# Optimization experiments

Measured on AMD Instinct MI355X. Metric: run time of the kernel, lower is better.

Reference implementation:

```python
import jax, jax.numpy as jnp
import numpy as np

EPS_ATT = 1e-6
EPS_BN = 1e-5


def setup_inputs() -> dict:
    key = jax.random.key(0)
    ks = jax.random.split(key, 12)
    B, Cin_half, H, W = 16, 128, 96, 96
    Cin, Cout, Cqk = 2 * Cin_half, 256, 256 // 8
    inp = {
        'fsp': jax.random.normal(ks[0], (B, Cin_half, H, W), jnp.float32),
        'fcp': jax.random.normal(ks[1], (B, Cin_half, H, W), jnp.float32),
        # 1x1 conv of ConvBNReLU (bias=False): store as [out, in]
        'conv_w': jax.random.normal(ks[2], (Cout, Cin), jnp.float32) * (1.0 / np.sqrt(Cin)),
        'bn_scale': jax.random.normal(ks[3], (Cout,), jnp.float32) * 0.1 + 1.0,
        'bn_bias': jax.random.normal(ks[4], (Cout,), jnp.float32) * 0.1,
        'bn_mean': jax.random.normal(ks[5], (Cout,), jnp.float32) * 0.1,
        'bn_var': jax.random.uniform(ks[6], (Cout,), jnp.float32, 0.5, 1.5),
        'gamma': jnp.ones((1,), jnp.float32) * 0.5,  # attention residual scale
        'q_w': jax.random.normal(ks[7], (Cqk, Cout), jnp.float32) * (1.0 / np.sqrt(Cout)),
        'q_b': jnp.zeros((Cqk,), jnp.float32),
        'k_w': jax.random.normal(ks[8], (Cqk, Cout), jnp.float32) * (1.0 / np.sqrt(Cout)),
        'k_b': jnp.zeros((Cqk,), jnp.float32),
        'v_w': jax.random.normal(ks[9], (Cout, Cout), jnp.float32) * (1.0 / np.sqrt(Cout)),
        'v_b': jnp.zeros((Cout,), jnp.float32),
    }
    return inp


def _l2_norm(x):
    # x: [B, C, N]; normalize over channel dim (dim=-2), matching torch l2_norm
    return x / jnp.linalg.norm(x, axis=-2, keepdims=True)


def reference(fsp, fcp, conv_w, bn_scale, bn_bias, bn_mean, bn_var,
              gamma, q_w, q_b, k_w, k_b, v_w, v_b):
    x = jnp.concatenate([fsp, fcp], axis=1)  # [B, Cin, H, W]
    # 1x1 conv + BN (eval, running stats) + ReLU
    feat = jnp.einsum('bchw,oc->bohw', x, conv_w)
    inv_std = jax.lax.rsqrt(bn_var + EPS_BN)
    feat = (feat - bn_mean[:, None, None]) * (bn_scale * inv_std)[:, None, None] + bn_bias[:, None, None]
    feat = jax.nn.relu(feat)

    B, C, H, W = feat.shape
    N = H * W
    f = feat.reshape(B, C, N)
    Q = jnp.einsum('bcn,oc->bon', f, q_w) + q_b[:, None]  # [B, Cq, N]
    K = jnp.einsum('bcn,oc->bon', f, k_w) + k_b[:, None]
    V = jnp.einsum('bcn,oc->bon', f, v_w) + v_b[:, None]  # [B, C, N]

    Qn = _l2_norm(Q).transpose(0, 2, 1)  # [B, N, Cq]
    Kn = _l2_norm(K)                     # [B, Cq, N]

    tailor = 1.0 / (N + jnp.einsum('bnc,bc->bn', Qn, jnp.sum(Kn, axis=-1) + EPS_ATT))  # [B, N]
    value_sum = jnp.sum(V, axis=-1)[:, :, None]          # [B, C, 1]
    matrix = jnp.einsum('bmn,bcn->bmc', Kn, V)           # [B, Cq, C]
    matrix_sum = value_sum + jnp.einsum('bnm,bmc->bcn', Qn, matrix)  # [B, C, N]
    weight_value = (matrix_sum * tailor[:, None, :]).reshape(B, C, H, W)

    atten = feat + gamma[0] * weight_value
    return feat * atten + feat
```

## Files before the change

### kernel.cpp

```cpp
#include <hip/hip_runtime.h>


typedef short short8 __attribute__((ext_vector_type(8)));
typedef __bf16 bf16x8 __attribute__((ext_vector_type(8)));
typedef float f32x4 __attribute__((ext_vector_type(4)));

#define DEVFN static __device__ __forceinline__

static constexpr int NB = 16;
static constexpr int C = 256;
static constexpr int HW = 9216;
static constexpr float FN = 9216.0f;
static constexpr float EPS_ATT_C = 1e-6f;
static constexpr float EPS_BN_C = 1e-5f;

DEVFN unsigned short f2b(float f) {
  unsigned u = __float_as_uint(f);
  u += 0x7FFFu + ((u >> 16) & 1u);
  return (unsigned short)(u >> 16);
}
DEVFN float b2f(unsigned short s) { return __uint_as_float(((unsigned)s) << 16); }

DEVFN float featval(float v) { return v; }
DEVFN float featval(unsigned short v) { return b2f(v); }
DEVFN short featbits(float v) { return (short)f2b(v); }
DEVFN short featbits(unsigned short v) { return (short)v; }
DEVFN void feat_store(float* p, float v) { *p = v; }
DEVFN void feat_store(unsigned short* p, float v) { *p = f2b(v); }

DEVFN f32x4 mfma16(short8 a, short8 b, f32x4 c) {
  return __builtin_amdgcn_mfma_f32_16x16x32_bf16(
      __builtin_bit_cast(bf16x8, a), __builtin_bit_cast(bf16x8, b), c, 0, 0, 0);
}

__global__ __launch_bounds__(256) void k_prep(
    const float* __restrict__ conv_w, const float* __restrict__ bn_scale,
    const float* __restrict__ bn_bias, const float* __restrict__ bn_mean,
    const float* __restrict__ bn_var, const float* __restrict__ q_w,
    const float* __restrict__ k_w, const float* __restrict__ v_w,
    unsigned short* __restrict__ Abf, float* __restrict__ biasA,
    unsigned short* __restrict__ qwbf, unsigned short* __restrict__ kwbf,
    float* __restrict__ vwT, float* __restrict__ fsum, float* __restrict__ Ksum,
    float* __restrict__ KF) {
  int tid = blockIdx.x * 256 + threadIdx.x;
  int nth = gridDim.x * 256;
  for (int i = tid; i < 65536; i += nth) {
    int o = i >> 8;
    float sc = bn_scale[o] * rsqrtf(bn_var[o] + EPS_BN_C);
    Abf[i] = f2b(conv_w[i] * sc);
  }
  for (int i = tid; i < 256; i += nth) {
    float sc = bn_scale[i] * rsqrtf(bn_var[i] + EPS_BN_C);
    biasA[i] = bn_bias[i] - bn_mean[i] * sc;
  }
  for (int i = tid; i < 8192; i += nth) {
    qwbf[i] = f2b(q_w[i]);
    kwbf[i] = f2b(k_w[i]);
  }
  for (int i = tid; i < 65536; i += nth) {
    int c = i >> 8, cp = i & 255;
    vwT[cp * 256 + c] = v_w[i];
  }
  for (int i = tid; i < NB * 256; i += nth) fsum[i] = 0.f;
  for (int i = tid; i < NB * 32; i += nth) Ksum[i] = 0.f;
  for (int i = tid; i < NB * 32 * 256; i += nth) KF[i] = 0.f;
}

template <typename FT>
__global__ __launch_bounds__(256) void k_conv(
    const float* __restrict__ fsp, const float* __restrict__ fcp,
    const unsigned short* __restrict__ Abf, const float* __restrict__ biasA,
    FT* __restrict__ feat, float* __restrict__ fsum) {
  const int b = blockIdx.y;
  const int p0 = blockIdx.x * 64;
  const int tid = threadIdx.x;
  const int w = tid >> 6, lane = tid & 63, g = lane >> 4, li = lane & 15;

  f32x4 acc[4][4];
#pragma unroll
  for (int i = 0; i < 4; ++i)
#pragma unroll
    for (int j = 0; j < 4; ++j) acc[i][j] = f32x4{0.f, 0.f, 0.f, 0.f};

  const short* Ab = (const short*)Abf;

#pragma unroll 1
  for (int kk = 0; kk < 256; kk += 32) {
    short8 af[4];
#pragma unroll
    for (int i = 0; i < 4; ++i) {
      int o = w * 64 + i * 16 + li;
      af[i] = *(const short8*)(Ab + o * 256 + kk + g * 8);
    }
    const float* src = (kk < 128) ? (fsp + ((size_t)b * 128 + kk) * HW)
                                  : (fcp + ((size_t)b * 128 + (kk - 128)) * HW);
    short8 bfr[4];
#pragma unroll
    for (int j = 0; j < 4; ++j) {
      const float* sp = src + (size_t)g * 8 * HW + p0 + j * 16 + li;
#pragma unroll
      for (int jj = 0; jj < 8; ++jj) bfr[j][jj] = (short)f2b(sp[(size_t)jj * HW]);
    }
#pragma unroll
    for (int i = 0; i < 4; ++i)
#pragma unroll
      for (int j = 0; j < 4; ++j)
        acc[i][j] = mfma16(af[i], bfr[j], acc[i][j]);
  }

  FT* fb = feat + (size_t)b * C * HW;
#pragma unroll
  for (int i = 0; i < 4; ++i) {
#pragma unroll
    for (int r = 0; r < 4; ++r) {
      int o = w * 64 + i * 16 + g * 4 + r;
      float bias = biasA[o];
      float s = 0.f;
#pragma unroll
      for (int j = 0; j < 4; ++j) {
        int p = p0 + j * 16 + li;
        float v = fmaxf(acc[i][j][r] + bias, 0.f);
        feat_store(&fb[(size_t)o * HW + p], v);
        s += v;
      }
      s += __shfl_xor(s, 1); s += __shfl_xor(s, 2);
      s += __shfl_xor(s, 4); s += __shfl_xor(s, 8);
      if (li == 0) atomicAdd(&fsum[b * 256 + o], s);
    }
  }
}

template <typename FT>
__global__ __launch_bounds__(256) void k_qk(
    const FT* __restrict__ feat, const unsigned short* __restrict__ qwbf,
    const unsigned short* __restrict__ kwbf, const float* __restrict__ q_b,
    const float* __restrict__ k_b, unsigned short* __restrict__ QnT,
    unsigned short* __restrict__ Kn, float* __restrict__ Ksum) {
  const int b = blockIdx.y;
  const int tid = threadIdx.x;
  const int w = tid >> 6, lane = tid & 63, g = lane >> 4, li = lane & 15;
  const int p0 = blockIdx.x * 256 + w * 64;

  const FT* fs = feat + (size_t)b * C * HW;
  const short* qw = (const short*)qwbf;
  const short* kw = (const short*)kwbf;

  f32x4 aq[4][2], ak[2][4];
#pragma unroll
  for (int t = 0; t < 4; ++t)
#pragma unroll
    for (int m = 0; m < 2; ++m) {
      aq[t][m] = f32x4{0.f, 0.f, 0.f, 0.f};
      ak[m][t] = f32x4{0.f, 0.f, 0.f, 0.f};
    }

#pragma unroll 1
  for (int kk = 0; kk < 256; kk += 32) {
    short8 ft[4];
#pragma unroll
    for (int t = 0; t < 4; ++t) {
      const FT* f8 = fs + (size_t)(kk + g * 8) * HW + p0 + t * 16 + li;
#pragma unroll
      for (int jj = 0; jj < 8; ++jj) ft[t][jj] = featbits(f8[(size_t)jj * HW]);
    }
    short8 qf[2], kf[2];
#pragma unroll
    for (int m = 0; m < 2; ++m) {
      qf[m] = *(const short8*)(qw + (m * 16 + li) * 256 + kk + g * 8);
      kf[m] = *(const short8*)(kw + (m * 16 + li) * 256 + kk + g * 8);
    }
#pragma unroll
    for (int t = 0; t < 4; ++t)
#pragma unroll
      for (int m = 0; m < 2; ++m)
        aq[t][m] = mfma16(ft[t], qf[m], aq[t][m]);
#pragma unroll
    for (int m = 0; m < 2; ++m)
#pragma unroll
      for (int t = 0; t < 4; ++t)
        ak[m][t] = mfma16(kf[m], ft[t], ak[m][t]);
  }

  float qb0 = q_b[li], qb1 = q_b[16 + li];
#pragma unroll
  for (int t = 0; t < 4; ++t) {
#pragma unroll
    for (int r = 0; r < 4; ++r) {
      float v0 = aq[t][0][r] + qb0;
      float v1 = aq[t][1][r] + qb1;
      float ss = v0 * v0 + v1 * v1;
      ss += __shfl_xor(ss, 1); ss += __shfl_xor(ss, 2);
      ss += __shfl_xor(ss, 4); ss += __shfl_xor(ss, 8);
      float sc = 1.0f / sqrtf(ss);
      int p = p0 + t * 16 + g * 4 + r;
      unsigned short* qp = QnT + ((size_t)b * HW + p) * 32;
      qp[li] = f2b(v0 * sc);
      qp[16 + li] = f2b(v1 * sc);
    }
  }

  float kb[2][4];
#pragma unroll
  for (int mi = 0; mi < 2; ++mi)
#pragma unroll
    for (int r = 0; r < 4; ++r) kb[mi][r] = k_b[mi * 16 + g * 4 + r];

  float ks[2][4];
#pragma unroll
  for (int mi = 0; mi < 2; ++mi)
#pragma unroll
    for (int r = 0; r < 4; ++r) ks[mi][r] = 0.f;

#pragma unroll
  for (int t = 0; t < 4; ++t) {
    float v[2][4];
    float ss = 0.f;
#pragma unroll
    for (int mi = 0; mi < 2; ++mi)
#pragma unroll
      for (int r = 0; r < 4; ++r) {
        v[mi][r] = ak[mi][t][r] + kb[mi][r];
        ss += v[mi][r] * v[mi][r];
      }
    ss += __shfl_xor(ss, 16); ss += __shfl_xor(ss, 32);
    float sc = 1.0f / sqrtf(ss);
    int p = p0 + t * 16 + li;
#pragma unroll
    for (int mi = 0; mi < 2; ++mi)
#pragma unroll
      for (int r = 0; r < 4; ++r) {
        float kn = v[mi][r] * sc;
        Kn[((size_t)b * 32 + mi * 16 + g * 4 + r) * HW + p] = f2b(kn);
        ks[mi][r] += kn;
      }
  }
#pragma unroll
  for (int mi = 0; mi < 2; ++mi)
#pragma unroll
    for (int r = 0; r < 4; ++r) {
      float s = ks[mi][r];
      s += __shfl_xor(s, 1); s += __shfl_xor(s, 2);
      s += __shfl_xor(s, 4); s += __shfl_xor(s, 8);
      if (li == 0) atomicAdd(&Ksum[b * 32 + mi * 16 + g * 4 + r], s);
    }
}

template <typename FT>
__global__ __launch_bounds__(256) void k_kf(
    const unsigned short* __restrict__ Kn, const FT* __restrict__ feat,
    float* __restrict__ KF) {
  const int b = blockIdx.y;
  const int n0 = blockIdx.x * 256;
  const int tid = threadIdx.x;
  const int w = tid >> 6, lane = tid & 63, g = lane >> 4, li = lane & 15;
  const short* kn = (const short*)Kn + (size_t)b * 32 * HW;
  const FT* fs = feat + (size_t)b * C * HW;

  f32x4 acc[2][4];
#pragma unroll
  for (int mi = 0; mi < 2; ++mi)
#pragma unroll
    for (int j = 0; j < 4; ++j) acc[mi][j] = f32x4{0.f, 0.f, 0.f, 0.f};

#pragma unroll 1
  for (int s = 0; s < 8; ++s) {
    int nn = n0 + s * 32;
    short8 a[2], bb[4];
#pragma unroll
    for (int mi = 0; mi < 2; ++mi)
      a[mi] = *(const short8*)(kn + (size_t)(mi * 16 + li) * HW + nn + g * 8);
#pragma unroll
    for (int j = 0; j < 4; ++j) {
      const FT* fp = fs + (size_t)(w * 64 + j * 16 + li) * HW + nn + g * 8;
      if constexpr (__is_same(FT, unsigned short)) {
        bb[j] = *(const short8*)fp;
      } else {
        f32x4 x0 = *(const f32x4*)fp;
        f32x4 x1 = *(const f32x4*)(fp + 4);
#pragma unroll
        for (int jj = 0; jj < 4; ++jj) {
          bb[j][jj] = (short)f2b(x0[jj]);
          bb[j][4 + jj] = (short)f2b(x1[jj]);
        }
      }
    }
#pragma unroll
    for (int mi = 0; mi < 2; ++mi)
#pragma unroll
      for (int j = 0; j < 4; ++j)
        acc[mi][j] = mfma16(a[mi], bb[j], acc[mi][j]);
  }
  float* kfp = KF + (size_t)b * 32 * 256;
#pragma unroll
  for (int mi = 0; mi < 2; ++mi)
#pragma unroll
    for (int j = 0; j < 4; ++j)
#pragma unroll
      for (int r = 0; r < 4; ++r) {
        int m = mi * 16 + g * 4 + r;
        int c = w * 64 + j * 16 + li;
        atomicAdd(&kfp[m * 256 + c], acc[mi][j][r]);
      }
}

__global__ __launch_bounds__(256) void k_mat(
    const float* __restrict__ KF, const float* __restrict__ vwT,
    const float* __restrict__ v_b, const float* __restrict__ fsum,
    const float* __restrict__ Ksum, unsigned short* __restrict__ matT,
    float* __restrict__ vsum, float* __restrict__ tsc) {
  __shared__ float kf_l[32 * 256];
  __shared__ float fs_l[256];
  __shared__ float ks_l[32];
  const int b = blockIdx.x;
  const int tid = threadIdx.x;
  for (int i = tid; i < 8192; i += 256) kf_l[i] = KF[b * 8192 + i];
  fs_l[tid] = fsum[b * 256 + tid];
  if (tid < 32) {
    float k0 = Ksum[b * 32 + tid];
    ks_l[tid] = k0;
    tsc[b * 32 + tid] = k0 + EPS_ATT_C;
  }
  __syncthreads();
  const int c = tid;
  float vs = 0.f;
  float mat[32];
#pragma unroll
  for (int m = 0; m < 32; ++m) mat[m] = 0.f;
  for (int cp = 0; cp < 256; ++cp) {
    float wv = vwT[cp * 256 + c];
    vs += wv * fs_l[cp];
#pragma unroll
    for (int m = 0; m < 32; ++m) mat[m] += wv * kf_l[m * 256 + cp];
  }
  float vb = v_b[c];
  vsum[b * 256 + c] = vs + FN * vb;
  unsigned short* mp = matT + ((size_t)b * 256 + c) * 32;
#pragma unroll
  for (int m = 0; m < 32; ++m) mp[m] = f2b(mat[m] + vb * ks_l[m]);
}

template <typename FT>
__global__ __launch_bounds__(256) void k_out(
    const FT* feat, const unsigned short* __restrict__ QnT,
    const unsigned short* __restrict__ matT, const float* __restrict__ vsum,
    const float* __restrict__ tsc, const float* __restrict__ gamma,
    float* out) {
  __shared__ float tail_l[64];
  __shared__ float vs_l[256];
  const int b = blockIdx.y;
  const int n0 = blockIdx.x * 64;
  const int tid = threadIdx.x;
  const int w = tid >> 6, lane = tid & 63, g = lane >> 4, li = lane & 15;
  const short* qn = (const short*)QnT + (size_t)b * HW * 32;

  vs_l[tid] = vsum[b * 256 + tid];
  if (tid < 64) {
    const short* qr = qn + (size_t)(n0 + tid) * 32;
    float d = 0.f;
#pragma unroll
    for (int m = 0; m < 32; ++m) d += b2f((unsigned short)qr[m]) * tsc[b * 32 + m];
    tail_l[tid] = 1.0f / (FN + d);
  }
  __syncthreads();

  const short* mt = (const short*)matT + (size_t)b * 256 * 32;
  short8 am[4], bq[4];
#pragma unroll
  for (int i = 0; i < 4; ++i)
    am[i] = *(const short8*)(mt + (w * 64 + i * 16 + li) * 32 + g * 8);
#pragma unroll
  for (int j = 0; j < 4; ++j)
    bq[j] = *(const short8*)(qn + (size_t)(n0 + j * 16 + li) * 32 + g * 8);

  f32x4 acc[4][4];
#pragma unroll
  for (int i = 0; i < 4; ++i)
#pragma unroll
    for (int j = 0; j < 4; ++j) {
      f32x4 z = f32x4{0.f, 0.f, 0.f, 0.f};
      acc[i][j] = mfma16(am[i], bq[j], z);
    }

  const float gam = gamma[0];
  const FT* fb = feat + (size_t)b * C * HW;
  float* ob = out + (size_t)b * C * HW;
#pragma unroll
  for (int i = 0; i < 4; ++i) {
#pragma unroll
    for (int r = 0; r < 4; ++r) {
      int c = w * 64 + i * 16 + g * 4 + r;
      float vsc = vs_l[c];
#pragma unroll
      for (int j = 0; j < 4; ++j) {
        int nl = j * 16 + li;
        float ms = acc[i][j][r] + vsc;
        float wv = tail_l[nl] * ms;
        float f = featval(fb[(size_t)c * HW + n0 + nl]);
        ob[(size_t)c * HW + n0 + nl] = f * (f + gam * wv + 1.0f);
      }
    }
  }
}

extern "C" void kernel_launch(void* const* d_in, const int* in_sizes, int n_in,
                              void* d_out, int out_size, void* d_ws, size_t ws_size,
                              hipStream_t stream) {
  const float* fsp = (const float*)d_in[0];
  const float* fcp = (const float*)d_in[1];
  const float* conv_w = (const float*)d_in[2];
  const float* bn_scale = (const float*)d_in[3];
  const float* bn_bias = (const float*)d_in[4];
  const float* bn_mean = (const float*)d_in[5];
  const float* bn_var = (const float*)d_in[6];
  const float* gamma = (const float*)d_in[7];
  const float* q_w = (const float*)d_in[8];
  const float* q_b = (const float*)d_in[9];
  const float* k_w = (const float*)d_in[10];
  const float* k_b = (const float*)d_in[11];
  const float* v_w = (const float*)d_in[12];
  const float* v_b = (const float*)d_in[13];

  char* ws = (char*)d_ws;
  size_t off = 0;
  auto alloc = [&](size_t bytes) {
    off = (off + 255) & ~(size_t)255;
    void* p = ws + off;
    off += bytes;
    return p;
  };
  const size_t featBytesBf16 = (size_t)NB * C * HW * 2;
  unsigned short* featB = (unsigned short*)alloc(featBytesBf16);
  unsigned short* QnT  = (unsigned short*)alloc((size_t)NB * HW * 32 * 2);
  unsigned short* Kn   = (unsigned short*)alloc((size_t)NB * 32 * HW * 2);
  unsigned short* Abf  = (unsigned short*)alloc(65536 * 2);
  float* biasA = (float*)alloc(256 * 4);
  unsigned short* qwbf = (unsigned short*)alloc(8192 * 2);
  unsigned short* kwbf = (unsigned short*)alloc(8192 * 2);
  float* vwT  = (float*)alloc(65536 * 4);
  float* fsum = (float*)alloc(NB * 256 * 4);
  float* Ksum = (float*)alloc(NB * 32 * 4);
  float* tsc  = (float*)alloc(NB * 32 * 4);
  float* KF   = (float*)alloc((size_t)NB * 32 * 256 * 4);
  unsigned short* matT = (unsigned short*)alloc((size_t)NB * 256 * 32 * 2);
  float* vsum = (float*)alloc(NB * 256 * 4);
  const bool bf16path = (off <= ws_size);
  if (!bf16path) {
    off = 0;
    QnT  = (unsigned short*)alloc((size_t)NB * HW * 32 * 2);
    Kn   = (unsigned short*)alloc((size_t)NB * 32 * HW * 2);
    Abf  = (unsigned short*)alloc(65536 * 2);
    biasA = (float*)alloc(256 * 4);
    qwbf = (unsigned short*)alloc(8192 * 2);
    kwbf = (unsigned short*)alloc(8192 * 2);
    vwT  = (float*)alloc(65536 * 4);
    fsum = (float*)alloc(NB * 256 * 4);
    Ksum = (float*)alloc(NB * 32 * 4);
    tsc  = (float*)alloc(NB * 32 * 4);
    KF   = (float*)alloc((size_t)NB * 32 * 256 * 4);
    matT = (unsigned short*)alloc((size_t)NB * 256 * 32 * 2);
    vsum = (float*)alloc(NB * 256 * 4);
  }
  float* featF = (float*)d_out;
  float* out = (float*)d_out;

  k_prep<<<dim3(64), dim3(256), 0, stream>>>(conv_w, bn_scale, bn_bias, bn_mean,
                                             bn_var, q_w, k_w, v_w, Abf, biasA,
                                             qwbf, kwbf, vwT, fsum, Ksum, KF);
  if (bf16path) {
    k_conv<unsigned short><<<dim3(144, 16), dim3(256), 0, stream>>>(fsp, fcp, Abf, biasA, featB, fsum);
    k_qk<unsigned short><<<dim3(36, 16), dim3(256), 0, stream>>>(featB, qwbf, kwbf, q_b, k_b, QnT, Kn, Ksum);
    k_kf<unsigned short><<<dim3(36, 16), dim3(256), 0, stream>>>(Kn, featB, KF);
    k_mat<<<dim3(16), dim3(256), 0, stream>>>(KF, vwT, v_b, fsum, Ksum, matT, vsum, tsc);
    k_out<unsigned short><<<dim3(144, 16), dim3(256), 0, stream>>>(featB, QnT, matT, vsum, tsc, gamma, out);
  } else {
    k_conv<float><<<dim3(144, 16), dim3(256), 0, stream>>>(fsp, fcp, Abf, biasA, featF, fsum);
    k_qk<float><<<dim3(36, 16), dim3(256), 0, stream>>>(featF, qwbf, kwbf, q_b, k_b, QnT, Kn, Ksum);
    k_kf<float><<<dim3(36, 16), dim3(256), 0, stream>>>(Kn, featF, KF);
    k_mat<<<dim3(16), dim3(256), 0, stream>>>(KF, vwT, v_b, fsum, Ksum, matT, vsum, tsc);
    k_out<float><<<dim3(144, 16), dim3(256), 0, stream>>>(featF, QnT, matT, vsum, tsc, gamma, out);
  }
}
```

Before: 493.9 us.

## Stage conv and QK input tiles through LDS, use MFMA for value projection

k_conv and k_qk now load their channel-major input tiles with coalesced vector reads, convert them to bf16 and transpose them into a double-buffered padded LDS tile. Previously each lane issued eight strided scalar loads per fragment. k_mat replaces its scalar 32-wide FMA loop over the fp32 transposed value weights with bf16 MFMA tiles over a bf16 copy of v_w, so k_prep no longer transposes v_w. This lowers global load inefficiency in the large kernels and compute time in the single-wave-per-batch k_mat. In exchange it adds a barrier per K step, extra LDS traffic, and bf16 rounding of the value weights and KF.

```diff
diff --git a/kernel.cpp b/kernel.cpp
--- a/kernel.cpp
+++ b/kernel.cpp
@@ -13,6 +13,7 @@
 static constexpr float FN = 9216.0f;
 static constexpr float EPS_ATT_C = 1e-6f;
 static constexpr float EPS_BN_C = 1e-5f;
+static constexpr int LSTR = 40;
 
 DEVFN unsigned short f2b(float f) {
   unsigned u = __float_as_uint(f);
@@ -23,8 +24,6 @@
 
 DEVFN float featval(float v) { return v; }
 DEVFN float featval(unsigned short v) { return b2f(v); }
-DEVFN short featbits(float v) { return (short)f2b(v); }
-DEVFN short featbits(unsigned short v) { return (short)v; }
 DEVFN void feat_store(float* p, float v) { *p = v; }
 DEVFN void feat_store(unsigned short* p, float v) { *p = f2b(v); }
 
@@ -40,8 +39,8 @@
     const float* __restrict__ k_w, const float* __restrict__ v_w,
     unsigned short* __restrict__ Abf, float* __restrict__ biasA,
     unsigned short* __restrict__ qwbf, unsigned short* __restrict__ kwbf,
-    float* __restrict__ vwT, float* __restrict__ fsum, float* __restrict__ Ksum,
-    float* __restrict__ KF) {
+    unsigned short* __restrict__ vwbf, float* __restrict__ fsum,
+    float* __restrict__ Ksum, float* __restrict__ KF) {
   int tid = blockIdx.x * 256 + threadIdx.x;
   int nth = gridDim.x * 256;
   for (int i = tid; i < 65536; i += nth) {
@@ -57,10 +56,7 @@
     qwbf[i] = f2b(q_w[i]);
     kwbf[i] = f2b(k_w[i]);
   }
-  for (int i = tid; i < 65536; i += nth) {
-    int c = i >> 8, cp = i & 255;
-    vwT[cp * 256 + c] = v_w[i];
-  }
+  for (int i = tid; i < 65536; i += nth) vwbf[i] = f2b(v_w[i]);
   for (int i = tid; i < NB * 256; i += nth) fsum[i] = 0.f;
   for (int i = tid; i < NB * 32; i += nth) Ksum[i] = 0.f;
   for (int i = tid; i < NB * 32 * 256; i += nth) KF[i] = 0.f;
@@ -71,10 +67,12 @@
     const float* __restrict__ fsp, const float* __restrict__ fcp,
     const unsigned short* __restrict__ Abf, const float* __restrict__ biasA,
     FT* __restrict__ feat, float* __restrict__ fsum) {
+  __shared__ unsigned short xl[2][64 * LSTR];
   const int b = blockIdx.y;
   const int p0 = blockIdx.x * 64;
   const int tid = threadIdx.x;
   const int w = tid >> 6, lane = tid & 63, g = lane >> 4, li = lane & 15;
+  const int sc = tid & 31, spg = tid >> 5;
 
   f32x4 acc[4][4];
 #pragma unroll
@@ -86,21 +84,27 @@
 
 #pragma unroll 1
   for (int kk = 0; kk < 256; kk += 32) {
+    const int ks = (kk >> 5) & 1;
+    const float* src = (kk < 128)
+        ? (fsp + ((size_t)b * 128 + kk + sc) * HW)
+        : (fcp + ((size_t)b * 128 + (kk - 128) + sc) * HW);
+    f32x4 x0 = *(const f32x4*)(src + p0 + spg * 8);
+    f32x4 x1 = *(const f32x4*)(src + p0 + spg * 8 + 4);
+    unsigned short* dst = &xl[ks][(spg * 8) * LSTR + sc];
+#pragma unroll
+    for (int i = 0; i < 4; ++i) dst[i * LSTR] = f2b(x0[i]);
+#pragma unroll
+    for (int i = 0; i < 4; ++i) dst[(4 + i) * LSTR] = f2b(x1[i]);
+    __syncthreads();
+
     short8 af[4];
 #pragma unroll
-    for (int i = 0; i < 4; ++i) {
-      int o = w * 64 + i * 16 + li;
-      af[i] = *(const short8*)(Ab + o * 256 + kk + g * 8);
-    }
-    const float* src = (kk < 128) ? (fsp + ((size_t)b * 128 + kk) * HW)
-                                  : (fcp + ((size_t)b * 128 + (kk - 128)) * HW);
+    for (int i = 0; i < 4; ++i)
+      af[i] = *(const short8*)(Ab + (w * 64 + i * 16 + li) * 256 + kk + g * 8);
     short8 bfr[4];
 #pragma unroll
-    for (int j = 0; j < 4; ++j) {
-      const float* sp = src + (size_t)g * 8 * HW + p0 + j * 16 + li;
-#pragma unroll
-      for (int jj = 0; jj < 8; ++jj) bfr[j][jj] = (short)f2b(sp[(size_t)jj * HW]);
-    }
+    for (int j = 0; j < 4; ++j)
+      bfr[j] = *(const short8*)&xl[ks][(j * 16 + li) * LSTR + g * 8];
 #pragma unroll
     for (int i = 0; i < 4; ++i)
 #pragma unroll
@@ -136,10 +140,13 @@
     const unsigned short* __restrict__ kwbf, const float* __restrict__ q_b,
     const float* __restrict__ k_b, unsigned short* __restrict__ QnT,
     unsigned short* __restrict__ Kn, float* __restrict__ Ksum) {
+  __shared__ unsigned short fl[2][256 * LSTR];
   const int b = blockIdx.y;
   const int tid = threadIdx.x;
   const int w = tid >> 6, lane = tid & 63, g = lane >> 4, li = lane & 15;
-  const int p0 = blockIdx.x * 256 + w * 64;
+  const int p0b = blockIdx.x * 256;
+  const int p0 = p0b + w * 64;
+  const int sc = tid & 31, spg = tid >> 5;
 
   const FT* fs = feat + (size_t)b * C * HW;
   const short* qw = (const short*)qwbf;
@@ -156,13 +163,30 @@
 
 #pragma unroll 1
   for (int kk = 0; kk < 256; kk += 32) {
+    const int ks = (kk >> 5) & 1;
+    const FT* srow = fs + (size_t)(kk + sc) * HW + p0b + spg * 32;
+    unsigned short* dst = &fl[ks][(spg * 32) * LSTR + sc];
+    if constexpr (__is_same(FT, unsigned short)) {
+#pragma unroll
+      for (int q = 0; q < 4; ++q) {
+        short8 v = *(const short8*)((const short*)srow + q * 8);
+#pragma unroll
+        for (int i = 0; i < 8; ++i) dst[(q * 8 + i) * LSTR] = (unsigned short)v[i];
+      }
+    } else {
+#pragma unroll
+      for (int q = 0; q < 8; ++q) {
+        f32x4 v = *(const f32x4*)((const float*)srow + q * 4);
+#pragma unroll
+        for (int i = 0; i < 4; ++i) dst[(q * 4 + i) * LSTR] = f2b(v[i]);
+      }
+    }
+    __syncthreads();
+
     short8 ft[4];
 #pragma unroll
-    for (int t = 0; t < 4; ++t) {
-      const FT* f8 = fs + (size_t)(kk + g * 8) * HW + p0 + t * 16 + li;
-#pragma unroll
-      for (int jj = 0; jj < 8; ++jj) ft[t][jj] = featbits(f8[(size_t)jj * HW]);
-    }
+    for (int t = 0; t < 4; ++t)
+      ft[t] = *(const short8*)&fl[ks][(w * 64 + t * 16 + li) * LSTR + g * 8];
     short8 qf[2], kf[2];
 #pragma unroll
     for (int m = 0; m < 2; ++m) {
@@ -191,11 +215,11 @@
       float ss = v0 * v0 + v1 * v1;
       ss += __shfl_xor(ss, 1); ss += __shfl_xor(ss, 2);
       ss += __shfl_xor(ss, 4); ss += __shfl_xor(ss, 8);
-      float sc = 1.0f / sqrtf(ss);
+      float sc2 = 1.0f / sqrtf(ss);
       int p = p0 + t * 16 + g * 4 + r;
       unsigned short* qp = QnT + ((size_t)b * HW + p) * 32;
-      qp[li] = f2b(v0 * sc);
-      qp[16 + li] = f2b(v1 * sc);
+      qp[li] = f2b(v0 * sc2);
+      qp[16 + li] = f2b(v1 * sc2);
     }
   }
 
@@ -205,11 +229,11 @@
 #pragma unroll
     for (int r = 0; r < 4; ++r) kb[mi][r] = k_b[mi * 16 + g * 4 + r];
 
-  float ks[2][4];
+  float ksum_r[2][4];
 #pragma unroll
   for (int mi = 0; mi < 2; ++mi)
 #pragma unroll
-    for (int r = 0; r < 4; ++r) ks[mi][r] = 0.f;
+    for (int r = 0; r < 4; ++r) ksum_r[mi][r] = 0.f;
 
 #pragma unroll
   for (int t = 0; t < 4; ++t) {
@@ -223,22 +247,22 @@
         ss += v[mi][r] * v[mi][r];
       }
     ss += __shfl_xor(ss, 16); ss += __shfl_xor(ss, 32);
-    float sc = 1.0f / sqrtf(ss);
+    float sc2 = 1.0f / sqrtf(ss);
     int p = p0 + t * 16 + li;
 #pragma unroll
     for (int mi = 0; mi < 2; ++mi)
 #pragma unroll
       for (int r = 0; r < 4; ++r) {
-        float kn = v[mi][r] * sc;
+        float kn = v[mi][r] * sc2;
         Kn[((size_t)b * 32 + mi * 16 + g * 4 + r) * HW + p] = f2b(kn);
-        ks[mi][r] += kn;
+        ksum_r[mi][r] += kn;
       }
   }
 #pragma unroll
   for (int mi = 0; mi < 2; ++mi)
 #pragma unroll
     for (int r = 0; r < 4; ++r) {
-      float s = ks[mi][r];
+      float s = ksum_r[mi][r];
       s += __shfl_xor(s, 1); s += __shfl_xor(s, 2);
       s += __shfl_xor(s, 4); s += __shfl_xor(s, 8);
       if (li == 0) atomicAdd(&Ksum[b * 32 + mi * 16 + g * 4 + r], s);
@@ -304,39 +328,73 @@
 }
 
 __global__ __launch_bounds__(256) void k_mat(
-    const float* __restrict__ KF, const float* __restrict__ vwT,
+    const float* __restrict__ KF, const unsigned short* __restrict__ vwbf,
     const float* __restrict__ v_b, const float* __restrict__ fsum,
     const float* __restrict__ Ksum, unsigned short* __restrict__ matT,
     float* __restrict__ vsum, float* __restrict__ tsc) {
-  __shared__ float kf_l[32 * 256];
   __shared__ float fs_l[256];
-  __shared__ float ks_l[32];
   const int b = blockIdx.x;
   const int tid = threadIdx.x;
-  for (int i = tid; i < 8192; i += 256) kf_l[i] = KF[b * 8192 + i];
+  const int w = tid >> 6, lane = tid & 63, g = lane >> 4, li = lane & 15;
   fs_l[tid] = fsum[b * 256 + tid];
-  if (tid < 32) {
-    float k0 = Ksum[b * 32 + tid];
-    ks_l[tid] = k0;
-    tsc[b * 32 + tid] = k0 + EPS_ATT_C;
-  }
+  if (tid < 32) tsc[b * 32 + tid] = Ksum[b * 32 + tid] + EPS_ATT_C;
   __syncthreads();
-  const int c = tid;
-  float vs = 0.f;
-  float mat[32];
-#pragma unroll
-  for (int m = 0; m < 32; ++m) mat[m] = 0.f;
-  for (int cp = 0; cp < 256; ++cp) {
-    float wv = vwT[cp * 256 + c];
-    vs += wv * fs_l[cp];
-#pragma unroll
-    for (int m = 0; m < 32; ++m) mat[m] += wv * kf_l[m * 256 + cp];
-  }
-  float vb = v_b[c];
-  vsum[b * 256 + c] = vs + FN * vb;
-  unsigned short* mp = matT + ((size_t)b * 256 + c) * 32;
-#pragma unroll
-  for (int m = 0; m < 32; ++m) mp[m] = f2b(mat[m] + vb * ks_l[m]);
+
+  const short* vw = (const short*)vwbf;
+  const float* kfb = KF + (size_t)b * 8192;
+
+  f32x4 acc[4][2];
+#pragma unroll
+  for (int i = 0; i < 4; ++i)
+#pragma unroll
+    for (int jm = 0; jm < 2; ++jm) acc[i][jm] = f32x4{0.f, 0.f, 0.f, 0.f};
+
+#pragma unroll 1
+  for (int kk = 0; kk < 256; kk += 32) {
+    short8 af[4];
+#pragma unroll
+    for (int i = 0; i < 4; ++i)
+      af[i] = *(const short8*)(vw + (w * 64 + i * 16 + li) * 256 + kk + g * 8);
+    short8 bf[2];
+#pragma unroll
+    for (int jm = 0; jm < 2; ++jm) {
+      const float* kp = kfb + (jm * 16 + li) * 256 + kk + g * 8;
+      f32x4 x0 = *(const f32x4*)kp;
+      f32x4 x1 = *(const f32x4*)(kp + 4);
+#pragma unroll
+      for (int jj = 0; jj < 4; ++jj) {
+        bf[jm][jj] = (short)f2b(x0[jj]);
+        bf[jm][4 + jj] = (short)f2b(x1[jj]);
+      }
+    }
+#pragma unroll
+    for (int i = 0; i < 4; ++i)
+#pragma unroll
+      for (int jm = 0; jm < 2; ++jm)
+        acc[i][jm] = mfma16(af[i], bf[jm], acc[i][jm]);
+  }
+
+  {
+    const int c = tid;
+    float vs = 0.f;
+    for (int cp = 0; cp < 256; ++cp)
+      vs += b2f((unsigned short)vw[c * 256 + cp]) * fs_l[cp];
+    vsum[b * 256 + c] = vs + FN * v_b[c];
+  }
+
+  float ks0 = Ksum[b * 32 + li];
+  float ks1 = Ksum[b * 32 + 16 + li];
+#pragma unroll
+  for (int i = 0; i < 4; ++i) {
+#pragma unroll
+    for (int r = 0; r < 4; ++r) {
+      int cc = w * 64 + i * 16 + g * 4 + r;
+      float vb = v_b[cc];
+      unsigned short* mp = matT + ((size_t)b * 256 + cc) * 32;
+      mp[li] = f2b(acc[i][0][r] + vb * ks0);
+      mp[16 + li] = f2b(acc[i][1][r] + vb * ks1);
+    }
+  }
 }
 
 template <typename FT>
@@ -436,7 +494,7 @@
   float* biasA = (float*)alloc(256 * 4);
   unsigned short* qwbf = (unsigned short*)alloc(8192 * 2);
   unsigned short* kwbf = (unsigned short*)alloc(8192 * 2);
-  float* vwT  = (float*)alloc(65536 * 4);
+  unsigned short* vwbf = (unsigned short*)alloc(65536 * 2);
   float* fsum = (float*)alloc(NB * 256 * 4);
   float* Ksum = (float*)alloc(NB * 32 * 4);
   float* tsc  = (float*)alloc(NB * 32 * 4);
@@ -452,7 +510,7 @@
     biasA = (float*)alloc(256 * 4);
     qwbf = (unsigned short*)alloc(8192 * 2);
     kwbf = (unsigned short*)alloc(8192 * 2);
-    vwT  = (float*)alloc(65536 * 4);
+    vwbf = (unsigned short*)alloc(65536 * 2);
     fsum = (float*)alloc(NB * 256 * 4);
     Ksum = (float*)alloc(NB * 32 * 4);
     tsc  = (float*)alloc(NB * 32 * 4);
@@ -465,18 +523,18 @@
 
   k_prep<<<dim3(64), dim3(256), 0, stream>>>(conv_w, bn_scale, bn_bias, bn_mean,
                                              bn_var, q_w, k_w, v_w, Abf, biasA,
-                                             qwbf, kwbf, vwT, fsum, Ksum, KF);
+                                             qwbf, kwbf, vwbf, fsum, Ksum, KF);
   if (bf16path) {
     k_conv<unsigned short><<<dim3(144, 16), dim3(256), 0, stream>>>(fsp, fcp, Abf, biasA, featB, fsum);
     k_qk<unsigned short><<<dim3(36, 16), dim3(256), 0, stream>>>(featB, qwbf, kwbf, q_b, k_b, QnT, Kn, Ksum);
     k_kf<unsigned short><<<dim3(36, 16), dim3(256), 0, stream>>>(Kn, featB, KF);
-    k_mat<<<dim3(16), dim3(256), 0, stream>>>(KF, vwT, v_b, fsum, Ksum, matT, vsum, tsc);
+    k_mat<<<dim3(16), dim3(256), 0, stream>>>(KF, vwbf, v_b, fsum, Ksum, matT, vsum, tsc);
     k_out<unsigned short><<<dim3(144, 16), dim3(256), 0, stream>>>(featB, QnT, matT, vsum, tsc, gamma, out);
   } else {
     k_conv<float><<<dim3(144, 16), dim3(256), 0, stream>>>(fsp, fcp, Abf, biasA, featF, fsum);
     k_qk<float><<<dim3(36, 16), dim3(256), 0, stream>>>(featF, qwbf, kwbf, q_b, k_b, QnT, Kn, Ksum);
     k_kf<float><<<dim3(36, 16), dim3(256), 0, stream>>>(Kn, featF, KF);
-    k_mat<<<dim3(16), dim3(256), 0, stream>>>(KF, vwT, v_b, fsum, Ksum, matT, vsum, tsc);
+    k_mat<<<dim3(16), dim3(256), 0, stream>>>(KF, vwbf, v_b, fsum, Ksum, matT, vsum, tsc);
     k_out<float><<<dim3(144, 16), dim3(256), 0, stream>>>(featF, QnT, matT, vsum, tsc, gamma, out);
   }
 }
```

Measured after the change: 453.2 us. -8.2%, faster.
